# Performance work log

Hardware: AMD Instinct MI355X
Metric: run time of the kernel (lower is better)

The kernel has to match this reference:

```python
import jax, jax.numpy as jnp
import numpy as np

N, E, IN, HID, HEADS, OUT = 20000, 320000, 128, 64, 8, 64
NEG_SLOPE = 0.2  # PyG GATConv default leaky_relu slope


def setup_inputs() -> dict:
    key = jax.random.key(0)
    ks = jax.random.split(key, 12)
    g = lambda k, shape, fan_in: jax.random.normal(k, shape, jnp.float32) / np.sqrt(fan_in)
    return {
        "x": jax.random.normal(ks[0], (N, IN), jnp.float32),
        "edge_index": jax.random.randint(ks[1], (2, E), 0, N, jnp.int32),
        "W1": g(ks[2], (IN, HEADS * HID), IN),
        "att_src1": g(ks[3], (HEADS, HID), HID),
        "att_dst1": g(ks[4], (HEADS, HID), HID),
        "b1": jnp.zeros((HEADS * HID,), jnp.float32),
        "W2": g(ks[5], (HEADS * HID, OUT), HEADS * HID),
        "att_src2": g(ks[6], (1, OUT), OUT),
        "att_dst2": g(ks[7], (1, OUT), OUT),
        "b2": jnp.zeros((OUT,), jnp.float32),
    }


def gat_conv(x, edge_index, W, att_src, att_dst, b, heads, out_ch):
    """PyG-style GATConv with add_self_loops=True, concat=True."""
    n = x.shape[0]
    loop = jnp.arange(n, dtype=edge_index.dtype)
    src = jnp.concatenate([edge_index[0], loop])  # message source nodes
    dst = jnp.concatenate([edge_index[1], loop])  # aggregation targets

    h = (x @ W).reshape(n, heads, out_ch)               # [N,H,C]
    a_s = jnp.sum(h * att_src[None], axis=-1)            # [N,H]
    a_d = jnp.sum(h * att_dst[None], axis=-1)            # [N,H]

    e = jax.nn.leaky_relu(a_s[src] + a_d[dst], NEG_SLOPE)  # [Etot,H]
    # numerically stable edge-softmax over incoming neighborhoods
    m = jax.ops.segment_max(e, dst, num_segments=n)
    m = jnp.where(jnp.isfinite(m), m, 0.0)
    p = jnp.exp(e - m[dst])
    denom = jax.ops.segment_sum(p, dst, num_segments=n)
    alpha = p / denom[dst]                               # [Etot,H]

    out = jax.ops.segment_sum(h[src] * alpha[:, :, None], dst, num_segments=n)  # [N,H,C]
    return out.reshape(n, heads * out_ch) + b


def reference(x, edge_index, W1, att_src1, att_dst1, b1, W2, att_src2, att_dst2, b2):
    h = gat_conv(x, edge_index, W1, att_src1, att_dst1, b1, HEADS, HID)
    h = jax.nn.relu(h)
    out = gat_conv(h, edge_index, W2, att_src2, att_dst2, b2, 1, OUT)
    return out
```

## Files before the change

kernel.cpp:

```cpp
#include <hip/hip_runtime.h>
#include <cstdint>

#define N_NODES 20000
#define N_EDGES 320000
#define ET (N_EDGES + N_NODES)
#define IN_DIM 128
#define HID 64
#define HEADS 8
#define F1 (HEADS * HID)
#define OUT_DIM 64
#define NEG_SLOPE 0.2f
#define NB_SCAN 20

typedef __attribute__((ext_vector_type(8))) short bf16x8;
typedef __attribute__((ext_vector_type(4))) float f32x4;

__device__ __forceinline__ ushort f2bf(float f) {
  uint32_t u = __float_as_uint(f);
  uint32_t r = (u + 0x7fffu + ((u >> 16) & 1u)) >> 16;
  return (ushort)r;
}
__device__ __forceinline__ float bfu_lo(uint32_t p) { return __uint_as_float(p << 16); }
__device__ __forceinline__ float bfu_hi(uint32_t p) { return __uint_as_float(p & 0xffff0000u); }
__device__ __forceinline__ float lrelu(float x) { return x > 0.f ? x : NEG_SLOPE * x; }

__global__ void prep_kernel(const float* __restrict__ x, const float* __restrict__ W1,
                            const float* __restrict__ W2, ushort* __restrict__ xb,
                            ushort* __restrict__ W1T, ushort* __restrict__ W2T) {
  const int NX4 = N_NODES * IN_DIM / 4;
  int idx = blockIdx.x * 256 + threadIdx.x;
  if (idx < NX4) {
    float4 v = reinterpret_cast<const float4*>(x)[idx];
    ushort4 o;
    o.x = f2bf(v.x); o.y = f2bf(v.y); o.z = f2bf(v.z); o.w = f2bf(v.w);
    reinterpret_cast<ushort4*>(xb)[idx] = o;
  } else if (idx < NX4 + IN_DIM * F1) {
    int k = idx - NX4;
    int r = k / F1, c = k - r * F1;
    W1T[(size_t)c * IN_DIM + r] = f2bf(W1[k]);
  } else if (idx < NX4 + IN_DIM * F1 + F1 * OUT_DIM) {
    int k = idx - NX4 - IN_DIM * F1;
    int r = k / OUT_DIM, c = k - r * OUT_DIM;
    W2T[(size_t)c * F1 + r] = f2bf(W2[k]);
  }
}

__global__ void hist_kernel(const int* __restrict__ ei, int* __restrict__ deg) {
  int e = blockIdx.x * 256 + threadIdx.x;
  if (e >= ET) return;
  int dst = (e < N_EDGES) ? ei[N_EDGES + e] : (e - N_EDGES);
  atomicAdd(&deg[dst], 1);
}

__global__ __launch_bounds__(1024) void scan_a(const int* __restrict__ deg,
                                               int* __restrict__ off,
                                               int* __restrict__ bsum) {
  __shared__ int wsum[16];
  int i = blockIdx.x * 1024 + threadIdx.x;
  int lane = threadIdx.x & 63, wid = threadIdx.x >> 6;
  int v = (i < N_NODES) ? deg[i] : 0;
  int s = v;
#pragma unroll
  for (int d = 1; d < 64; d <<= 1) {
    int u = __shfl_up(s, d);
    if (lane >= d) s += u;
  }
  if (lane == 63) wsum[wid] = s;
  __syncthreads();
  if (wid == 0) {
    int ws = (lane < 16) ? wsum[lane] : 0;
#pragma unroll
    for (int d = 1; d < 16; d <<= 1) {
      int u = __shfl_up(ws, d);
      if (lane >= d) ws += u;
    }
    if (lane < 16) wsum[lane] = ws;
  }
  __syncthreads();
  int wbase = (wid > 0) ? wsum[wid - 1] : 0;
  int incl = wbase + s;
  if (i < N_NODES) off[i] = incl - v;
  if (threadIdx.x == 1023) bsum[blockIdx.x] = incl;
}

__global__ void scan_b(const int* __restrict__ bsum, int* __restrict__ boff,
                       int* __restrict__ off) {
  int lane = threadIdx.x;
  int orig = (lane < NB_SCAN) ? bsum[lane] : 0;
  int v = orig;
#pragma unroll
  for (int d = 1; d < 64; d <<= 1) {
    int u = __shfl_up(v, d);
    if (lane >= d) v += u;
  }
  if (lane < NB_SCAN) boff[lane] = v - orig;
  if (lane == NB_SCAN - 1) off[N_NODES] = v;
}

__global__ __launch_bounds__(1024) void scan_c(const int* __restrict__ boff,
                                               int* __restrict__ off,
                                               int* __restrict__ pos) {
  int i = blockIdx.x * 1024 + threadIdx.x;
  if (i >= N_NODES) return;
  int o = off[i] + boff[blockIdx.x];
  off[i] = o;
  pos[i] = o;
}

__global__ void scatter_kernel(const int* __restrict__ ei, int* __restrict__ pos,
                               int* __restrict__ csr_src) {
  int e = blockIdx.x * 256 + threadIdx.x;
  if (e >= ET) return;
  int src, dst;
  if (e < N_EDGES) { src = ei[e]; dst = ei[N_EDGES + e]; }
  else             { src = e - N_EDGES; dst = src; }
  int slot = atomicAdd(&pos[dst], 1);
  csr_src[slot] = src;
}

__device__ __forceinline__ int swz(int r, int kg) { return kg ^ ((r >> 1) & 3); }

template <int WR, int WC, int TM, int TN, int ASD>
__global__ __launch_bounds__(256) void gemm_kernel(
    const ushort* __restrict__ A, const ushort* __restrict__ BT,
    ushort* __restrict__ Cb, int M, int K, int NC,
    const float* __restrict__ atts, const float* __restrict__ attd,
    float* __restrict__ asd) {
  constexpr int BM = WR * TM * 16;
  constexpr int BN = WC * TN * 16;
  __shared__ ushort As[BM * 32];
  __shared__ ushort Bs[BN * 32];
  const int t = threadIdx.x;
  const int lane = t & 63, wid = t >> 6;
  const int wr = wid / WC, wc = wid % WC;
  const int m0 = blockIdx.y * BM, n0 = blockIdx.x * BN;
  f32x4 acc[TM][TN] = {};
  const int srow = t >> 2, kg = t & 3;

  for (int k0 = 0; k0 < K; k0 += 32) {
#pragma unroll
    for (int q = 0; q < BM / 64; ++q) {
      int r = srow + 64 * q;
      int gr = m0 + r; if (gr >= M) gr = M - 1;
      bf16x8 v = *reinterpret_cast<const bf16x8*>(&A[(size_t)gr * K + k0 + kg * 8]);
      *reinterpret_cast<bf16x8*>(&As[r * 32 + swz(r, kg) * 8]) = v;
    }
#pragma unroll
    for (int q = 0; q < BN / 64; ++q) {
      int r = srow + 64 * q;
      int gn = n0 + r;
      bf16x8 v = *reinterpret_cast<const bf16x8*>(&BT[(size_t)gn * K + k0 + kg * 8]);
      *reinterpret_cast<bf16x8*>(&Bs[r * 32 + swz(r, kg) * 8]) = v;
    }
    __syncthreads();
    int kq = lane >> 4;
    int rr = lane & 15;
    bf16x8 af[TM], bfv[TN];
#pragma unroll
    for (int i = 0; i < TM; ++i) {
      int r = (wr * TM + i) * 16 + rr;
      af[i] = *reinterpret_cast<const bf16x8*>(&As[r * 32 + swz(r, kq) * 8]);
    }
#pragma unroll
    for (int j = 0; j < TN; ++j) {
      int r = (wc * TN + j) * 16 + rr;
      bfv[j] = *reinterpret_cast<const bf16x8*>(&Bs[r * 32 + swz(r, kq) * 8]);
    }
#pragma unroll
    for (int i = 0; i < TM; ++i)
#pragma unroll
      for (int j = 0; j < TN; ++j)
        acc[i][j] = __builtin_amdgcn_mfma_f32_16x16x32_bf16(af[i], bfv[j], acc[i][j], 0, 0, 0);
    __syncthreads();
  }
  const int cr0 = (lane >> 4) * 4;
  const int cc = lane & 15;
#pragma unroll
  for (int i = 0; i < TM; ++i)
#pragma unroll
    for (int j = 0; j < TN; ++j)
#pragma unroll
      for (int r = 0; r < 4; ++r) {
        int gm = m0 + (wr * TM + i) * 16 + cr0 + r;
        int gn = n0 + (wc * TN + j) * 16 + cc;
        if (gm < M) Cb[(size_t)gm * NC + gn] = f2bf(acc[i][j][r]);
      }
  if constexpr (ASD != 0) {
    static_assert(TN * 16 == 64, "asd fusion needs 64-col wave tile");
    const int hh = (ASD == 1) ? ((n0 + wc * 64) >> 6) : 0;
    float as_v[TN], ad_v[TN];
#pragma unroll
    for (int j = 0; j < TN; ++j) {
      as_v[j] = atts[hh * 64 + j * 16 + cc];
      ad_v[j] = attd[hh * 64 + j * 16 + cc];
    }
#pragma unroll
    for (int i = 0; i < TM; ++i)
#pragma unroll
      for (int r = 0; r < 4; ++r) {
        float ps = 0.f, pd = 0.f;
#pragma unroll
        for (int j = 0; j < TN; ++j) {
          ps += acc[i][j][r] * as_v[j];
          pd += acc[i][j][r] * ad_v[j];
        }
#pragma unroll
        for (int s = 1; s < 16; s <<= 1) {
          ps += __shfl_xor(ps, s);
          pd += __shfl_xor(pd, s);
        }
        int row = m0 + (wr * TM + i) * 16 + cr0 + r;
        if (cc == 0 && row < M) {
          if constexpr (ASD == 1) {
            asd[(size_t)row * 16 + hh] = ps;
            asd[(size_t)row * 16 + 8 + hh] = pd;
          } else {
            asd[(size_t)row * 2 + 0] = ps;
            asd[(size_t)row * 2 + 1] = pd;
          }
        }
      }
  }
}

__global__ __launch_bounds__(64) void agg1_kernel(
    const int* __restrict__ off, const int* __restrict__ csrs,
    const float* __restrict__ asd, const ushort* __restrict__ H1b,
    const float* __restrict__ b1, ushort* __restrict__ X2b) {
  int bid = blockIdx.x;
  int head = bid & 7;
  int nb = bid >> 3;
  int lane = threadIdx.x;
  int grp = lane >> 4, fr = lane & 15;
  int gb = grp << 4;
  int node = nb * 4 + grp;
  int s0 = off[node], s1 = off[node + 1];
  float adst = asd[(size_t)node * 16 + 8 + head];
  const uint2* Hh = reinterpret_cast<const uint2*>(H1b) + head * 16 + fr;
  float m = -1e30f, s = 0.f;
  float a0 = 0.f, a1 = 0.f, a2 = 0.f, a3 = 0.f;
  for (int c0 = s0; c0 < s1; c0 += 16) {
    int nn = s1 - c0; if (nn > 16) nn = 16;
    int src_f = (fr < nn) ? csrs[c0 + fr] : 0;
    float e = (fr < nn) ? lrelu(asd[(size_t)src_f * 16 + head] + adst) : -1e30f;
    float mc = e;
#pragma unroll
    for (int d = 1; d < 16; d <<= 1) mc = fmaxf(mc, __shfl_xor(mc, d));
    float mn = fmaxf(m, mc);
    float wv = (fr < nn) ? __expf(e - mn) : 0.f;
    float ws = wv;
#pragma unroll
    for (int d = 1; d < 16; d <<= 1) ws += __shfl_xor(ws, d);
    float r = __expf(m - mn);
    s = s * r + ws;
    a0 *= r; a1 *= r; a2 *= r; a3 *= r;
    m = mn;
    int i = 0;
    for (; i + 2 <= nn; i += 2) {
      int sA = __shfl(src_f, gb + i);
      int sB = __shfl(src_f, gb + i + 1);
      float wA = __shfl(wv, gb + i);
      float wB = __shfl(wv, gb + i + 1);
      uint2 pA = Hh[(size_t)sA * 128];
      uint2 pB = Hh[(size_t)sB * 128];
      a0 += wA * bfu_lo(pA.x) + wB * bfu_lo(pB.x);
      a1 += wA * bfu_hi(pA.x) + wB * bfu_hi(pB.x);
      a2 += wA * bfu_lo(pA.y) + wB * bfu_lo(pB.y);
      a3 += wA * bfu_hi(pA.y) + wB * bfu_hi(pB.y);
    }
    if (i < nn) {
      int sA = __shfl(src_f, gb + i);
      float wA = __shfl(wv, gb + i);
      uint2 p = Hh[(size_t)sA * 128];
      a0 += wA * bfu_lo(p.x); a1 += wA * bfu_hi(p.x);
      a2 += wA * bfu_lo(p.y); a3 += wA * bfu_hi(p.y);
    }
  }
  float inv = 1.f / s;
  int fb = head * 64 + fr * 4;
  float v0 = fmaxf(a0 * inv + b1[fb], 0.f);
  float v1 = fmaxf(a1 * inv + b1[fb + 1], 0.f);
  float v2 = fmaxf(a2 * inv + b1[fb + 2], 0.f);
  float v3 = fmaxf(a3 * inv + b1[fb + 3], 0.f);
  uint2 o;
  o.x = (uint32_t)f2bf(v0) | ((uint32_t)f2bf(v1) << 16);
  o.y = (uint32_t)f2bf(v2) | ((uint32_t)f2bf(v3) << 16);
  reinterpret_cast<uint2*>(X2b)[(size_t)node * 128 + head * 16 + fr] = o;
}

__global__ __launch_bounds__(256) void agg2_kernel(
    const int* __restrict__ off, const int* __restrict__ csrs,
    const float* __restrict__ asd, const ushort* __restrict__ H2b,
    const float* __restrict__ b2, float* __restrict__ out) {
  __shared__ float w_lds[4][64];
  __shared__ int src_lds[4][64];
  int wv_id = threadIdx.x >> 6;
  int node = blockIdx.x * 4 + wv_id;
  if (node >= N_NODES) return;
  int lane = threadIdx.x & 63;
  int grp = lane >> 4, fr = lane & 15;
  int s0 = off[node], s1 = off[node + 1];
  float adst = asd[(size_t)node * 2 + 1];
  const uint2* Hp = reinterpret_cast<const uint2*>(H2b);
  float m = -1e30f, s = 0.f;
  float a0 = 0.f, a1 = 0.f, a2 = 0.f, a3 = 0.f;
  for (int c0 = s0; c0 < s1; c0 += 64) {
    int n = s1 - c0; if (n > 64) n = 64;
    int src = (lane < n) ? csrs[c0 + lane] : 0;
    float e = (lane < n) ? lrelu(asd[(size_t)src * 2] + adst) : -1e30f;
    float mc = e;
#pragma unroll
    for (int d = 1; d < 64; d <<= 1) mc = fmaxf(mc, __shfl_xor(mc, d));
    float mn = fmaxf(m, mc);
    float wv = (lane < n) ? __expf(e - mn) : 0.f;
    float ws = wv;
#pragma unroll
    for (int d = 1; d < 64; d <<= 1) ws += __shfl_xor(ws, d);
    float r = __expf(m - mn);
    s = s * r + ws;
    a0 *= r; a1 *= r; a2 *= r; a3 *= r;
    m = mn;
    src_lds[wv_id][lane] = src;
    w_lds[wv_id][lane] = wv;
    int i = grp;
    for (; i + 4 < n; i += 8) {
      int sA = src_lds[wv_id][i], sB = src_lds[wv_id][i + 4];
      float wA = w_lds[wv_id][i], wB = w_lds[wv_id][i + 4];
      uint2 pA = Hp[(size_t)sA * 16 + fr];
      uint2 pB = Hp[(size_t)sB * 16 + fr];
      a0 += wA * bfu_lo(pA.x) + wB * bfu_lo(pB.x);
      a1 += wA * bfu_hi(pA.x) + wB * bfu_hi(pB.x);
      a2 += wA * bfu_lo(pA.y) + wB * bfu_lo(pB.y);
      a3 += wA * bfu_hi(pA.y) + wB * bfu_hi(pB.y);
    }
    if (i < n) {
      int sA = src_lds[wv_id][i];
      float wA = w_lds[wv_id][i];
      uint2 p = Hp[(size_t)sA * 16 + fr];
      a0 += wA * bfu_lo(p.x); a1 += wA * bfu_hi(p.x);
      a2 += wA * bfu_lo(p.y); a3 += wA * bfu_hi(p.y);
    }
  }
#pragma unroll
  for (int d = 16; d < 64; d <<= 1) {
    a0 += __shfl_xor(a0, d);
    a1 += __shfl_xor(a1, d);
    a2 += __shfl_xor(a2, d);
    a3 += __shfl_xor(a3, d);
  }
  if (grp == 0) {
    float inv = 1.f / s;
    int fb = fr * 4;
    float4 o;
    o.x = a0 * inv + b2[fb];
    o.y = a1 * inv + b2[fb + 1];
    o.z = a2 * inv + b2[fb + 2];
    o.w = a3 * inv + b2[fb + 3];
    reinterpret_cast<float4*>(out)[(size_t)node * 16 + fr] = o;
  }
}

extern "C" void kernel_launch(void* const* d_in, const int* in_sizes, int n_in,
                              void* d_out, int out_size, void* d_ws, size_t ws_size,
                              hipStream_t stream) {
  const float* x        = (const float*)d_in[0];
  const int*   ei       = (const int*)  d_in[1];
  const float* W1       = (const float*)d_in[2];
  const float* att_src1 = (const float*)d_in[3];
  const float* att_dst1 = (const float*)d_in[4];
  const float* b1       = (const float*)d_in[5];
  const float* W2       = (const float*)d_in[6];
  const float* att_src2 = (const float*)d_in[7];
  const float* att_dst2 = (const float*)d_in[8];
  const float* b2       = (const float*)d_in[9];
  float* out = (float*)d_out;

  char* w = (char*)d_ws;
  auto alloc = [&](size_t bytes) {
    char* p = w;
    w += (bytes + 255) & ~(size_t)255;
    return p;
  };
  ushort* xb     = (ushort*)alloc((size_t)N_NODES * IN_DIM * 2);
  ushort* W1T    = (ushort*)alloc((size_t)F1 * IN_DIM * 2);
  ushort* W2T    = (ushort*)alloc((size_t)OUT_DIM * F1 * 2);
  ushort* H1b    = (ushort*)alloc((size_t)N_NODES * F1 * 2);
  ushort* X2b    = (ushort*)alloc((size_t)N_NODES * F1 * 2);
  ushort* H2b    = (ushort*)alloc((size_t)N_NODES * OUT_DIM * 2);
  float* asd1    = (float*)alloc((size_t)N_NODES * 16 * 4);
  float* asd2    = (float*)alloc((size_t)N_NODES * 2 * 4);
  int* deg       = (int*)alloc((size_t)N_NODES * 4);
  int* off       = (int*)alloc((size_t)(N_NODES + 1) * 4);
  int* pos       = (int*)alloc((size_t)N_NODES * 4);
  int* csrsrc    = (int*)alloc((size_t)ET * 4);
  int* bsum      = (int*)alloc((size_t)NB_SCAN * 4);
  int* boff      = (int*)alloc((size_t)NB_SCAN * 4);

  hipMemsetAsync(deg, 0, (size_t)N_NODES * 4, stream);
  hist_kernel<<<(ET + 255) / 256, 256, 0, stream>>>(ei, deg);
  scan_a<<<NB_SCAN, 1024, 0, stream>>>(deg, off, bsum);
  scan_b<<<1, 64, 0, stream>>>(bsum, boff, off);
  scan_c<<<NB_SCAN, 1024, 0, stream>>>(boff, off, pos);
  scatter_kernel<<<(ET + 255) / 256, 256, 0, stream>>>(ei, pos, csrsrc);

  {
    int total = N_NODES * IN_DIM / 4 + IN_DIM * F1 + F1 * OUT_DIM;
    prep_kernel<<<(total + 255) / 256, 256, 0, stream>>>(x, W1, W2, xb, W1T, W2T);
  }

  gemm_kernel<2, 2, 4, 4, 1>
      <<<dim3(F1 / 128, (N_NODES + 127) / 128), 256, 0, stream>>>(
      xb, W1T, H1b, N_NODES, IN_DIM, F1, att_src1, att_dst1, asd1);
  agg1_kernel<<<HEADS * (N_NODES / 4), 64, 0, stream>>>(off, csrsrc, asd1, H1b, b1, X2b);

  gemm_kernel<4, 1, 1, 4, 2>
      <<<dim3(1, (N_NODES + 63) / 64), 256, 0, stream>>>(
      X2b, W2T, H2b, N_NODES, F1, OUT_DIM, att_src2, att_dst2, asd2);
  agg2_kernel<<<(N_NODES + 3) / 4, 256, 0, stream>>>(off, csrsrc, asd2, H2b, b2, out);
}
```

Baseline: 143.7 us.

## Split layer-1 aggregation into separate edge-softmax and weighted-gather kernels

Replaces the fused online-softmax aggregation for layer 1 with a dedicated kernel that computes normalized attention weights per edge and head into a new workspace buffer. A simpler aggregation kernel then gathers one bf16 feature per lane with four-way unrolled loads, using one 64-lane wave per (node, head). This removes the per-chunk shuffles and rescaling from the gather loop, but adds an extra launch and a roughly 10 MB alpha write and read, and scalar 2-byte gathers instead of 8-byte vector loads.

```diff
diff --git a/kernel.cpp b/kernel.cpp
--- a/kernel.cpp
+++ b/kernel.cpp
@@ -19,6 +19,9 @@
   uint32_t u = __float_as_uint(f);
   uint32_t r = (u + 0x7fffu + ((u >> 16) & 1u)) >> 16;
   return (ushort)r;
+}
+__device__ __forceinline__ float bf2f(ushort u) {
+  return __uint_as_float((uint32_t)u << 16);
 }
 __device__ __forceinline__ float bfu_lo(uint32_t p) { return __uint_as_float(p << 16); }
 __device__ __forceinline__ float bfu_hi(uint32_t p) { return __uint_as_float(p & 0xffff0000u); }
@@ -223,69 +226,65 @@
   }
 }
 
-__global__ __launch_bounds__(64) void agg1_kernel(
+__global__ void alpha1_kernel(const int* __restrict__ off, const int* __restrict__ csrs,
+                              const float* __restrict__ asd, float* __restrict__ alpha) {
+  int node = blockIdx.x * 4 + (threadIdx.x >> 6);
+  if (node >= N_NODES) return;
+  int lane = threadIdx.x & 63;
+  int h = lane & 7;
+  int j = lane >> 3;
+  int s0 = off[node], s1 = off[node + 1];
+  float adst = asd[(size_t)node * 16 + 8 + h];
+  float mx = -1e30f;
+  for (int i = s0 + j; i < s1; i += 8) {
+    float xv = asd[(size_t)csrs[i] * 16 + h] + adst;
+    mx = fmaxf(mx, lrelu(xv));
+  }
+#pragma unroll
+  for (int s = 8; s < 64; s <<= 1) mx = fmaxf(mx, __shfl_xor(mx, s));
+  float sum = 0.f;
+  for (int i = s0 + j; i < s1; i += 8) {
+    float xv = lrelu(asd[(size_t)csrs[i] * 16 + h] + adst);
+    sum += __expf(xv - mx);
+  }
+#pragma unroll
+  for (int s = 8; s < 64; s <<= 1) sum += __shfl_xor(sum, s);
+  float inv = 1.f / sum;
+  for (int i = s0 + j; i < s1; i += 8) {
+    float xv = lrelu(asd[(size_t)csrs[i] * 16 + h] + adst);
+    alpha[(size_t)h * ET + i] = __expf(xv - mx) * inv;
+  }
+}
+
+__global__ __launch_bounds__(256) void agg1_kernel(
     const int* __restrict__ off, const int* __restrict__ csrs,
-    const float* __restrict__ asd, const ushort* __restrict__ H1b,
+    const float* __restrict__ alpha,
+    const ushort* __restrict__ H1b,
     const float* __restrict__ b1, ushort* __restrict__ X2b) {
-  int bid = blockIdx.x;
-  int head = bid & 7;
-  int nb = bid >> 3;
-  int lane = threadIdx.x;
-  int grp = lane >> 4, fr = lane & 15;
-  int gb = grp << 4;
-  int node = nb * 4 + grp;
+  int b = blockIdx.x;
+  int head = b & 7;
+  int nq = b >> 3;
+  int node = nq * 4 + (threadIdx.x >> 6);
+  node = __builtin_amdgcn_readfirstlane(node);
+  int lane = threadIdx.x & 63;
   int s0 = off[node], s1 = off[node + 1];
-  float adst = asd[(size_t)node * 16 + 8 + head];
-  const uint2* Hh = reinterpret_cast<const uint2*>(H1b) + head * 16 + fr;
-  float m = -1e30f, s = 0.f;
-  float a0 = 0.f, a1 = 0.f, a2 = 0.f, a3 = 0.f;
-  for (int c0 = s0; c0 < s1; c0 += 16) {
-    int nn = s1 - c0; if (nn > 16) nn = 16;
-    int src_f = (fr < nn) ? csrs[c0 + fr] : 0;
-    float e = (fr < nn) ? lrelu(asd[(size_t)src_f * 16 + head] + adst) : -1e30f;
-    float mc = e;
-#pragma unroll
-    for (int d = 1; d < 16; d <<= 1) mc = fmaxf(mc, __shfl_xor(mc, d));
-    float mn = fmaxf(m, mc);
-    float wv = (fr < nn) ? __expf(e - mn) : 0.f;
-    float ws = wv;
-#pragma unroll
-    for (int d = 1; d < 16; d <<= 1) ws += __shfl_xor(ws, d);
-    float r = __expf(m - mn);
-    s = s * r + ws;
-    a0 *= r; a1 *= r; a2 *= r; a3 *= r;
-    m = mn;
-    int i = 0;
-    for (; i + 2 <= nn; i += 2) {
-      int sA = __shfl(src_f, gb + i);
-      int sB = __shfl(src_f, gb + i + 1);
-      float wA = __shfl(wv, gb + i);
-      float wB = __shfl(wv, gb + i + 1);
-      uint2 pA = Hh[(size_t)sA * 128];
-      uint2 pB = Hh[(size_t)sB * 128];
-      a0 += wA * bfu_lo(pA.x) + wB * bfu_lo(pB.x);
-      a1 += wA * bfu_hi(pA.x) + wB * bfu_hi(pB.x);
-      a2 += wA * bfu_lo(pA.y) + wB * bfu_lo(pB.y);
-      a3 += wA * bfu_hi(pA.y) + wB * bfu_hi(pB.y);
-    }
-    if (i < nn) {
-      int sA = __shfl(src_f, gb + i);
-      float wA = __shfl(wv, gb + i);
-      uint2 p = Hh[(size_t)sA * 128];
-      a0 += wA * bfu_lo(p.x); a1 += wA * bfu_hi(p.x);
-      a2 += wA * bfu_lo(p.y); a3 += wA * bfu_hi(p.y);
-    }
-  }
-  float inv = 1.f / s;
-  int fb = head * 64 + fr * 4;
-  float v0 = fmaxf(a0 * inv + b1[fb], 0.f);
-  float v1 = fmaxf(a1 * inv + b1[fb + 1], 0.f);
-  float v2 = fmaxf(a2 * inv + b1[fb + 2], 0.f);
-  float v3 = fmaxf(a3 * inv + b1[fb + 3], 0.f);
-  uint2 o;
-  o.x = (uint32_t)f2bf(v0) | ((uint32_t)f2bf(v1) << 16);
-  o.y = (uint32_t)f2bf(v2) | ((uint32_t)f2bf(v3) << 16);
-  reinterpret_cast<uint2*>(X2b)[(size_t)node * 128 + head * 16 + fr] = o;
+  const ushort* Hh = H1b + head * 64 + lane;
+  const float* al = alpha + (size_t)head * ET;
+  float acc = 0.f;
+  int i = s0;
+  for (; i + 4 <= s1; i += 4) {
+    int sA = csrs[i], sB = csrs[i + 1], sC = csrs[i + 2], sD = csrs[i + 3];
+    float wA = al[i], wB = al[i + 1], wC = al[i + 2], wD = al[i + 3];
+    float vA = bf2f(Hh[(size_t)sA * 512]);
+    float vB = bf2f(Hh[(size_t)sB * 512]);
+    float vC = bf2f(Hh[(size_t)sC * 512]);
+    float vD = bf2f(Hh[(size_t)sD * 512]);
+    acc += wA * vA + wB * vB + wC * vC + wD * vD;
+  }
+  for (; i < s1; ++i)
+    acc += al[i] * bf2f(Hh[(size_t)csrs[i] * 512]);
+  float v = fmaxf(acc + b1[head * 64 + lane], 0.f);
+  X2b[(size_t)node * 512 + head * 64 + lane] = f2bf(v);
 }
 
 __global__ __launch_bounds__(256) void agg2_kernel(
@@ -389,6 +388,7 @@
   ushort* H2b    = (ushort*)alloc((size_t)N_NODES * OUT_DIM * 2);
   float* asd1    = (float*)alloc((size_t)N_NODES * 16 * 4);
   float* asd2    = (float*)alloc((size_t)N_NODES * 2 * 4);
+  float* alpha1  = (float*)alloc((size_t)ET * 8 * 4);
   int* deg       = (int*)alloc((size_t)N_NODES * 4);
   int* off       = (int*)alloc((size_t)(N_NODES + 1) * 4);
   int* pos       = (int*)alloc((size_t)N_NODES * 4);
@@ -411,7 +411,8 @@
   gemm_kernel<2, 2, 4, 4, 1>
       <<<dim3(F1 / 128, (N_NODES + 127) / 128), 256, 0, stream>>>(
       xb, W1T, H1b, N_NODES, IN_DIM, F1, att_src1, att_dst1, asd1);
-  agg1_kernel<<<HEADS * (N_NODES / 4), 64, 0, stream>>>(off, csrsrc, asd1, H1b, b1, X2b);
+  alpha1_kernel<<<(N_NODES + 3) / 4, 256, 0, stream>>>(off, csrsrc, asd1, alpha1);
+  agg1_kernel<<<HEADS * (N_NODES / 4), 256, 0, stream>>>(off, csrsrc, alpha1, H1b, b1, X2b);
 
   gemm_kernel<4, 1, 1, 4, 2>
       <<<dim3(1, (N_NODES + 63) / 64), 256, 0, stream>>>(
```

Measured after the change: 169.7 us. +18.1%, slower.
